# Optimization experiments

Hardware: AMD Instinct MI355X
Metric: run time of the kernel (lower is better)

## Reference

```python
import jax, jax.numpy as jnp
import numpy as np

N = 100000       # nodes
E = 1600000      # edges (avg degree 16)
F_IN = 128       # num_features
H = 128          # hidden
C = 10           # num_classes
L = 3            # num_layers
G = 128          # number of graphs in the batch


def setup_inputs() -> dict:
    key = jax.random.key(0)
    ks = jax.random.split(key, 12)
    x = jax.random.normal(ks[0], (N, F_IN), dtype=jnp.float32)
    edge_index = jax.random.randint(ks[1], (2, E), 0, N, dtype=jnp.int64)
    batch = jnp.sort(jax.random.randint(ks[2], (N,), 0, G, dtype=jnp.int64))
    def lin(k, fan_in, fan_out):
        s = 1.0 / np.sqrt(fan_in)
        return jax.random.uniform(k, (fan_in, fan_out), jnp.float32, -s, s)
    w_init = lin(ks[3], F_IN, H)
    b_init = jnp.zeros((H,), jnp.float32)
    w_conv = jnp.stack([lin(ks[4 + i], H, H) for i in range(L - 1)])  # [L-1,H,H]
    b_conv = jnp.zeros((L - 1, H), jnp.float32)
    w_h1 = lin(ks[8], H, H)
    b_h1 = jnp.zeros((H,), jnp.float32)
    w_h2 = lin(ks[9], H, C)
    b_h2 = jnp.zeros((C,), jnp.float32)
    return {"x": x, "edge_index": edge_index, "batch": batch,
            "w_init": w_init, "b_init": b_init,
            "w_conv": w_conv, "b_conv": b_conv,
            "w_h1": w_h1, "b_h1": b_h1, "w_h2": w_h2, "b_h2": b_h2}


def reference(x, edge_index, batch, w_init, b_init, w_conv, b_conv,
              w_h1, b_h1, w_h2, b_h2):
    n = x.shape[0]
    # GCNConv normalization: add self-loops, symmetric deg^-1/2 norm.
    loop = jnp.arange(n, dtype=edge_index.dtype)
    src = jnp.concatenate([edge_index[0], loop])
    dst = jnp.concatenate([edge_index[1], loop])
    deg = jax.ops.segment_sum(jnp.ones_like(dst, x.dtype), dst, num_segments=n)
    dinv = jnp.where(deg > 0, jax.lax.rsqrt(deg), 0.0)
    norm = dinv[src] * dinv[dst]  # [E+N]

    def gcn_conv(h, w, b):
        h = h @ w                                   # [N,H]
        msg = norm[:, None] * h[src]                # gather + scale
        return jax.ops.segment_sum(msg, dst, num_segments=n) + b

    h = jax.nn.relu(gcn_conv(x, w_init, b_init))
    for i in range(w_conv.shape[0]):
        h = jax.nn.relu(gcn_conv(h, w_conv[i], b_conv[i]))

    # global_mean_pool over graph ids
    sums = jax.ops.segment_sum(h, batch, num_segments=G)           # [G,H]
    cnt = jax.ops.segment_sum(jnp.ones((n,), h.dtype), batch, num_segments=G)
    pooled = sums / jnp.maximum(cnt, 1.0)[:, None]

    # classification head (dropout = identity at inference)
    h = jax.nn.relu(pooled @ w_h1 + b_h1)
    logits = h @ w_h2 + b_h2
    return jax.nn.log_softmax(logits, axis=-1)
```

## Files before the change

kernel.cpp:

```cpp
#include <hip/hip_runtime.h>
#include <hip/hip_bf16.h>
#include <math.h>

#define NN 100000
#define EE 1600000
#define HD 128
#define GG 128
#define CC 10

#define BKSH 9
#define NBK  196
#define CH   4096
#define MAXB 12288

typedef __attribute__((ext_vector_type(8))) short short8;
typedef __attribute__((ext_vector_type(4))) float f32x4;
typedef __attribute__((ext_vector_type(2))) float f32x2;

__device__ __forceinline__ unsigned short f2bf(float f) {
    union { float f; unsigned u; } a; a.f = f;
    unsigned r = a.u + 0x7fff + ((a.u >> 16) & 1);
    return (unsigned short)(r >> 16);
}
__device__ __forceinline__ float bfu(unsigned short u) {
    union { unsigned u; float f; } a; a.u = ((unsigned)u) << 16; return a.f;
}

__device__ __forceinline__ unsigned pk4fp8(float f0, float f1, float f2, float f3) {
    unsigned u = 0;
    u = __builtin_amdgcn_cvt_pk_fp8_f32(f0, f1, u, false);
    u = __builtin_amdgcn_cvt_pk_fp8_f32(f2, f3, u, true);
    return u;
}


__global__ __launch_bounds__(256) void k_bhist(const int* __restrict__ dst,
                                               unsigned* __restrict__ bucket_cnt) {
    __shared__ unsigned cnt[256];
    int t = threadIdx.x;
    cnt[t] = 0;
    __syncthreads();
    int base = blockIdx.x * CH;
#pragma unroll
    for (int k = 0; k < 16; ++k) {
        int e = base + k * 256 + t;
        if (e < EE) atomicAdd(&cnt[((unsigned)dst[e]) >> BKSH], 1u);
    }
    __syncthreads();
    if (cnt[t]) atomicAdd(&bucket_cnt[t], cnt[t]);
}

__global__ void k_bscan(const unsigned* __restrict__ bucket_cnt,
                        unsigned* __restrict__ bucket_start,
                        unsigned* __restrict__ cursor, int* __restrict__ row_start) {
    __shared__ unsigned s[256];
    int t = threadIdx.x;
    unsigned v = bucket_cnt[t];
    s[t] = v;
    __syncthreads();
    for (int off = 1; off < 256; off <<= 1) {
        unsigned a = (t >= off) ? s[t - off] : 0;
        __syncthreads();
        s[t] += a;
        __syncthreads();
    }
    unsigned excl = s[t] - v;
    bucket_start[t] = excl;
    cursor[t] = excl;
    if (t == 255) bucket_start[256] = excl + v;
    if (t == 0) row_start[NN] = EE;
}

__global__ __launch_bounds__(256) void k_bscatter(const int* __restrict__ src,
                                                  const int* __restrict__ dst,
                                                  unsigned* __restrict__ cursor,
                                                  unsigned* __restrict__ ebuf) {
    __shared__ unsigned cnt[256], lst[256], gbase[256], ss[256];
    __shared__ unsigned stage[CH];
    __shared__ unsigned char binid[CH];
    int t = threadIdx.x;
    cnt[t] = 0;
    __syncthreads();
    int base = blockIdx.x * CH;
    int nvalid = EE - base; if (nvalid > CH) nvalid = CH;

    unsigned bk[16], rk[16], pv[16];
#pragma unroll
    for (int k = 0; k < 16; ++k) {
        int e = base + k * 256 + t;
        bk[k] = 0xffffffffu;
        if (e < EE) {
            unsigned d = (unsigned)dst[e];
            unsigned b = d >> BKSH;
            pv[k] = (((unsigned)src[e]) << BKSH) | (d & ((1u << BKSH) - 1));
            bk[k] = b;
            rk[k] = atomicAdd(&cnt[b], 1u);
        }
    }
    __syncthreads();
    unsigned v = cnt[t];
    ss[t] = v;
    __syncthreads();
    for (int off = 1; off < 256; off <<= 1) {
        unsigned a = (t >= off) ? ss[t - off] : 0;
        __syncthreads();
        ss[t] += a;
        __syncthreads();
    }
    lst[t] = ss[t] - v;
    if (v) gbase[t] = atomicAdd(&cursor[t], v);
    __syncthreads();
#pragma unroll
    for (int k = 0; k < 16; ++k) {
        if (bk[k] != 0xffffffffu) {
            unsigned slot = lst[bk[k]] + rk[k];
            stage[slot] = pv[k];
            binid[slot] = (unsigned char)bk[k];
        }
    }
    __syncthreads();
    for (int j = t; j < nvalid; j += 256) {
        unsigned b = binid[j];
        ebuf[gbase[b] + (j - lst[b])] = stage[j];
    }
}

__global__ __launch_bounds__(1024) void k_bucket_csr(const unsigned* __restrict__ ebuf,
                                                     const unsigned* __restrict__ bucket_start,
                                                     int* __restrict__ row_start,
                                                     float* __restrict__ dinv,
                                                     int* __restrict__ col) {
    __shared__ unsigned degl[512], lst[512], lfill[512], ss[512];
    __shared__ int colstage[MAXB];
    int t = threadIdx.x, b = blockIdx.x;
    unsigned ebase = bucket_start[b];
    int size = (int)(bucket_start[b + 1] - ebase);
    int nbase = b << BKSH;
    if (t < 512) { degl[t] = 0; lfill[t] = 0; }
    __syncthreads();
    for (int j = t; j < size; j += 1024)
        atomicAdd(&degl[ebuf[ebase + j] & 511u], 1u);
    __syncthreads();
    unsigned v = 0;
    if (t < 512) { v = degl[t]; ss[t] = v; }
    __syncthreads();
    for (int off = 1; off < 512; off <<= 1) {
        unsigned a = 0;
        if (t < 512 && t >= off) a = ss[t - off];
        __syncthreads();
        if (t < 512) ss[t] += a;
        __syncthreads();
    }
    if (t < 512) {
        lst[t] = ss[t] - v;
        int node = nbase + t;
        if (node < NN) {
            row_start[node] = (int)(ebase + lst[t]);
            dinv[node] = rsqrtf((float)(v + 1));
        }
    }
    __syncthreads();
    if (size <= MAXB) {
        for (int j = t; j < size; j += 1024) {
            unsigned u = ebuf[ebase + j];
            unsigned l = u & 511u;
            unsigned pos = lst[l] + atomicAdd(&lfill[l], 1u);
            colstage[pos] = (int)(u >> BKSH);
        }
        __syncthreads();
        for (int j = t; j < size; j += 1024) col[ebase + j] = colstage[j];
    } else {
        for (int j = t; j < size; j += 1024) {
            unsigned u = ebuf[ebase + j];
            unsigned l = u & 511u;
            unsigned pos = lst[l] + atomicAdd(&lfill[l], 1u);
            col[ebase + pos] = (int)(u >> BKSH);
        }
    }
}


__global__ void k_prep_w(const float* __restrict__ w0, const float* __restrict__ w1,
                         const float* __restrict__ w2, unsigned short* __restrict__ Wt,
                         unsigned* __restrict__ bucket_cnt, float* __restrict__ pooled,
                         float* __restrict__ cntg) {
    int b = blockIdx.x;
    int t = threadIdx.x;
    if (b == 192) {
        bucket_cnt[t] = 0;
        for (int i = t; i < GG * HD; i += 256) pooled[i] = 0.f;
        if (t < GG) cntg[t] = 0.f;
        return;
    }
    int mat = b >> 6;
    int idx = (b & 63) * 256 + t;
    int k = idx >> 7, n = idx & 127;
    const float* Wm = (mat == 0) ? w0 : ((mat == 1) ? w1 : w2);
    Wt[mat * 16384 + n * 128 + k] = f2bf(Wm[k * 128 + n]);
}


#define LDK 136

template <bool F32IN>
__global__ __launch_bounds__(256) void k_gemm_mfma(
    const void* __restrict__ Ap, const unsigned short* __restrict__ Wt,
    const float* __restrict__ dinv, unsigned* __restrict__ g8) {
    __shared__ unsigned short As[128 * LDK];
    __shared__ unsigned short Ws[128 * LDK];
    __shared__ float dv[128];
    int t = threadIdx.x;
    int r0 = blockIdx.x * 128;

#pragma unroll
    for (int p = 0; p < 8; ++p) {
        int chunk = p * 256 + t;
        int row = chunk >> 4, kc = chunk & 15;
        uint4 sv = make_uint4(0u, 0u, 0u, 0u);
        if (F32IN) {
            const float* A = (const float*)Ap;
            if (r0 + row < NN) {
                const float* ap = A + (size_t)(r0 + row) * HD + kc * 8;
                float4 va = *(const float4*)ap;
                float4 vb = *(const float4*)(ap + 4);
                sv.x = (unsigned)f2bf(va.x) | ((unsigned)f2bf(va.y) << 16);
                sv.y = (unsigned)f2bf(va.z) | ((unsigned)f2bf(va.w) << 16);
                sv.z = (unsigned)f2bf(vb.x) | ((unsigned)f2bf(vb.y) << 16);
                sv.w = (unsigned)f2bf(vb.z) | ((unsigned)f2bf(vb.w) << 16);
            }
        } else {
            const unsigned short* A = (const unsigned short*)Ap;
            if (r0 + row < NN) sv = *(const uint4*)(A + (size_t)(r0 + row) * HD + kc * 8);
        }
        *(uint4*)(As + row * LDK + kc * 8) = sv;
        uint4 w = *(const uint4*)(Wt + (size_t)row * HD + kc * 8);
        *(uint4*)(Ws + row * LDK + kc * 8) = w;
    }
    if (t < 128) dv[t] = (r0 + t < NN) ? dinv[r0 + t] : 0.f;
    __syncthreads();

    int wave = t >> 6, lane = t & 63, quad = lane >> 4, l16 = lane & 15;
    int wr = (wave >> 1) * 64, wc = (wave & 1) * 64;

    f32x4 acc[4][4];
#pragma unroll
    for (int i = 0; i < 4; ++i)
#pragma unroll
        for (int j = 0; j < 4; ++j) acc[i][j] = (f32x4){0.f, 0.f, 0.f, 0.f};

#pragma unroll
    for (int kk = 0; kk < 4; ++kk) {
        int k0 = kk * 32 + quad * 8;
        short8 af[4], bfr[4];
#pragma unroll
        for (int i = 0; i < 4; ++i)
            af[i] = *(const short8*)(As + (wr + i * 16 + l16) * LDK + k0);
#pragma unroll
        for (int j = 0; j < 4; ++j)
            bfr[j] = *(const short8*)(Ws + (wc + j * 16 + l16) * LDK + k0);
#pragma unroll
        for (int i = 0; i < 4; ++i)
#pragma unroll
            for (int j = 0; j < 4; ++j)
                acc[i][j] = __builtin_amdgcn_mfma_f32_16x16x32_bf16(af[i], bfr[j], acc[i][j], 0, 0, 0);
    }
    __syncthreads();

#pragma unroll
    for (int i = 0; i < 4; ++i) {
        int lr = wr + i * 16 + quad * 4;
#pragma unroll
        for (int reg = 0; reg < 4; ++reg) {
            float sc = dv[lr + reg];
#pragma unroll
            for (int j = 0; j < 4; ++j)
                As[(lr + reg) * LDK + wc + j * 16 + l16] = f2bf(acc[i][j][reg] * sc);
        }
    }
    __syncthreads();

    int row = t >> 1, half = t & 1;
    if (r0 + row < NN) {
        const unsigned short* sp = As + row * LDK + half * 64;
        unsigned og[16];
#pragma unroll
        for (int q = 0; q < 16; ++q)
            og[q] = pk4fp8(bfu(sp[4 * q]), bfu(sp[4 * q + 1]),
                           bfu(sp[4 * q + 2]), bfu(sp[4 * q + 3]));
        uint4* dp = (uint4*)(g8 + (size_t)(r0 + row) * 32 + half * 16);
#pragma unroll
        for (int q = 0; q < 4; ++q)
            dp[q] = make_uint4(og[4 * q], og[4 * q + 1], og[4 * q + 2], og[4 * q + 3]);
    }
}


__global__ __launch_bounds__(256) void k_aggregate(
    const unsigned* __restrict__ g8, const int* __restrict__ row_start,
    const int* __restrict__ col, const float* __restrict__ dinv,
    const float* __restrict__ bias, uint2* __restrict__ out) {
    int node = blockIdx.x * 4 + (threadIdx.x >> 6);
    int lane = threadIdx.x & 63;
    int half = lane >> 5, l32 = lane & 31;

    f32x2 a01 = (f32x2){0.f, 0.f}, a23 = (f32x2){0.f, 0.f};
    {
        unsigned su = (half == 0) ? g8[node * 32 + l32] : 0u;
        a01 += __builtin_amdgcn_cvt_pk_f32_fp8(su, false);
        a23 += __builtin_amdgcn_cvt_pk_f32_fp8(su, true);
    }

    int e = row_start[node], end = row_start[node + 1];
    while (e < end) {
        int cnt = end - e; if (cnt > 64) cnt = 64;
        int li = lane < cnt ? lane : cnt - 1;
        int colv = col[e + li];
        int k = 0;
        for (; k + 16 <= cnt; k += 16) {
            unsigned u[8];
#pragma unroll
            for (int q = 0; q < 8; ++q) {
                int src = __builtin_amdgcn_ds_bpermute((k + q * 2 + half) << 2, colv);
                u[q] = g8[(unsigned)src * 32 + l32];
            }
#pragma unroll
            for (int q = 0; q < 8; ++q) {
                a01 += __builtin_amdgcn_cvt_pk_f32_fp8(u[q], false);
                a23 += __builtin_amdgcn_cvt_pk_f32_fp8(u[q], true);
            }
        }
        for (; k < cnt; k += 2) {
            int kk = k + half;
            bool valid = kk < cnt;
            int src = __builtin_amdgcn_ds_bpermute((valid ? kk : k) << 2, colv);
            unsigned u = g8[(unsigned)src * 32 + l32];
            if (!valid) u = 0u;
            a01 += __builtin_amdgcn_cvt_pk_f32_fp8(u, false);
            a23 += __builtin_amdgcn_cvt_pk_f32_fp8(u, true);
        }
        e += cnt;
    }

    a01.x += __shfl_down(a01.x, 32);
    a01.y += __shfl_down(a01.y, 32);
    a23.x += __shfl_down(a23.x, 32);
    a23.y += __shfl_down(a23.y, 32);

    if (half == 0) {
        float sc = dinv[node];
        float4 bb = ((const float4*)bias)[l32];
        float r0 = fmaxf(fmaf(a01.x, sc, bb.x), 0.f);
        float r1 = fmaxf(fmaf(a01.y, sc, bb.y), 0.f);
        float r2 = fmaxf(fmaf(a23.x, sc, bb.z), 0.f);
        float r3 = fmaxf(fmaf(a23.y, sc, bb.w), 0.f);
        uint2 o;
        o.x = (unsigned)f2bf(r0) | ((unsigned)f2bf(r1) << 16);
        o.y = (unsigned)f2bf(r2) | ((unsigned)f2bf(r3) << 16);
        out[node * 32 + l32] = o;
    }
}


__global__ __launch_bounds__(256) void k_pool_partial(
    const unsigned short* __restrict__ h, const int* __restrict__ batch,
    float* __restrict__ pooled, float* __restrict__ cntg) {
    int t = threadIdx.x;
    int slot = t >> 7, feat = t & 127;
    int base = blockIdx.x * 128;
    int endr = base + 128; if (endr > NN) endr = NN;
    float acc = 0.f;
    int cur = -1, run = 0;
    for (int r = base + slot; r < endr; r += 2) {
        int g = batch[r];
        float v = bfu(h[(size_t)r * HD + feat]);
        if (g != cur) {
            if (cur >= 0) {
                atomicAdd(&pooled[cur * HD + feat], acc);
                if (feat == 0) atomicAdd(&cntg[cur], (float)run);
            }
            cur = g; acc = 0.f; run = 0;
        }
        acc += v; ++run;
    }
    if (cur >= 0) {
        atomicAdd(&pooled[cur * HD + feat], acc);
        if (feat == 0) atomicAdd(&cntg[cur], (float)run);
    }
}


__global__ __launch_bounds__(128) void k_head(const float* __restrict__ pooled,
                                              const float* __restrict__ cntg,
                                              const float* __restrict__ w1,
                                              const float* __restrict__ b1,
                                              const float* __restrict__ w2,
                                              const float* __restrict__ b2,
                                              float* __restrict__ out) {
    __shared__ float row[HD], hrow[HD], logits[CC];
    int g = blockIdx.x, t = threadIdx.x;
    row[t] = pooled[g * HD + t] / fmaxf(cntg[g], 1.f);
    __syncthreads();
    float acc = b1[t];
    for (int k = 0; k < HD; ++k) acc = fmaf(row[k], w1[k * HD + t], acc);
    hrow[t] = fmaxf(acc, 0.f);
    __syncthreads();
    if (t < CC) {
        float a = b2[t];
        for (int k = 0; k < HD; ++k) a = fmaf(hrow[k], w2[k * CC + t], a);
        logits[t] = a;
    }
    __syncthreads();
    if (t < CC) {
        float m = logits[0];
        for (int i = 1; i < CC; ++i) m = fmaxf(m, logits[i]);
        float s = 0.f;
        for (int i = 0; i < CC; ++i) s += expf(logits[i] - m);
        out[g * CC + t] = logits[t] - m - logf(s);
    }
}


extern "C" void kernel_launch(void* const* d_in, const int* in_sizes, int n_in,
                              void* d_out, int out_size, void* d_ws, size_t ws_size,
                              hipStream_t stream) {
    const float* x      = (const float*)d_in[0];
    const int*   ei     = (const int*)d_in[1];
    const int*   batch  = (const int*)d_in[2];
    const float* w_init = (const float*)d_in[3];
    const float* b_init = (const float*)d_in[4];
    const float* w_conv = (const float*)d_in[5];
    const float* b_conv = (const float*)d_in[6];
    const float* w_h1   = (const float*)d_in[7];
    const float* b_h1   = (const float*)d_in[8];
    const float* w_h2   = (const float*)d_in[9];
    const float* b_h2   = (const float*)d_in[10];
    float* out = (float*)d_out;
    (void)n_in; (void)in_sizes; (void)out_size; (void)ws_size;

    char* ws = (char*)d_ws;
    size_t off = 0;
    auto alloc = [&](size_t bytes) -> void* {
        void* p = ws + off;
        off += (bytes + 255) & ~(size_t)255;
        return p;
    };
    unsigned short* hAbf         = (unsigned short*)alloc((size_t)NN * HD * 2);
    unsigned*       g8           = (unsigned*)alloc((size_t)NN * 32 * 4);
    unsigned short* Wt           = (unsigned short*)alloc(3 * 16384 * 2);
    float*          dinv         = (float*)alloc((size_t)NN * 4);
    int*            row_start    = (int*)alloc((size_t)(NN + 1) * 4);
    int*            col          = (int*)alloc((size_t)EE * 4);
    unsigned*       ebuf         = (unsigned*)alloc((size_t)EE * 4);
    unsigned*       bucket_cnt   = (unsigned*)alloc(256 * 4);
    unsigned*       bucket_start = (unsigned*)alloc(257 * 4);
    unsigned*       cursor       = (unsigned*)alloc(256 * 4);
    float*          pooled       = (float*)alloc((size_t)GG * HD * 4);
    float*          cntg         = (float*)alloc((size_t)GG * 4);

    const int* srcp = ei;
    const int* dstp = ei + EE;

    k_prep_w<<<193, 256, 0, stream>>>(w_init, w_conv, w_conv + HD * HD, Wt,
                                      bucket_cnt, pooled, cntg);

    int nchunks = (EE + CH - 1) / CH;
    k_bhist<<<nchunks, 256, 0, stream>>>(dstp, bucket_cnt);
    k_bscan<<<1, 256, 0, stream>>>(bucket_cnt, bucket_start, cursor, row_start);
    k_bscatter<<<nchunks, 256, 0, stream>>>(srcp, dstp, cursor, ebuf);
    k_bucket_csr<<<NBK, 1024, 0, stream>>>(ebuf, bucket_start, row_start, dinv, col);

    int gemm_grid = (NN + 127) / 128;
    int agg_grid = NN / 4;

    k_gemm_mfma<true><<<gemm_grid, 256, 0, stream>>>(x, Wt, dinv, g8);
    k_aggregate<<<agg_grid, 256, 0, stream>>>(g8, row_start, col, dinv, b_init, (uint2*)hAbf);
    k_gemm_mfma<false><<<gemm_grid, 256, 0, stream>>>(hAbf, Wt + 16384, dinv, g8);
    k_aggregate<<<agg_grid, 256, 0, stream>>>(g8, row_start, col, dinv, b_conv, (uint2*)hAbf);
    k_gemm_mfma<false><<<gemm_grid, 256, 0, stream>>>(hAbf, Wt + 2 * 16384, dinv, g8);
    k_aggregate<<<agg_grid, 256, 0, stream>>>(g8, row_start, col, dinv, b_conv + HD, (uint2*)hAbf);

    k_pool_partial<<<(NN + 127) / 128, 256, 0, stream>>>(hAbf, batch, pooled, cntg);
    k_head<<<GG, 128, 0, stream>>>(pooled, cntg, w_h1, b_h1, w_h2, b_h2, out);
}
```

Before: 389.8 us.

## Drop histogram pass with fixed-capacity buckets and use half-wave-per-node aggregation

Removes the separate destination histogram kernel by giving each bucket a fixed MAXB-sized slot in the edge buffer. The scatter advances per-bucket cursors from t*MAXB, and a scan afterwards derives compacted offsets from the final cursor values. The aggregation kernel now assigns 32 lanes per node (8 nodes per block) and walks edges serially in groups of 8 with prefetched column indices, replacing the wave-wide bpermute scheme and the cross-half reduction. This relies on no bucket exceeding MAXB edges; the overflow fallback path is removed.

```diff
diff --git a/kernel.cpp b/kernel.cpp
--- a/kernel.cpp
+++ b/kernel.cpp
@@ -34,42 +34,25 @@
 }
 
 
-__global__ __launch_bounds__(256) void k_bhist(const int* __restrict__ dst,
-                                               unsigned* __restrict__ bucket_cnt) {
-    __shared__ unsigned cnt[256];
+__global__ void k_prep_w(const float* __restrict__ w0, const float* __restrict__ w1,
+                         const float* __restrict__ w2, unsigned short* __restrict__ Wt,
+                         unsigned* __restrict__ cursor, float* __restrict__ pooled,
+                         float* __restrict__ cntg) {
+    int b = blockIdx.x;
     int t = threadIdx.x;
-    cnt[t] = 0;
-    __syncthreads();
-    int base = blockIdx.x * CH;
-#pragma unroll
-    for (int k = 0; k < 16; ++k) {
-        int e = base + k * 256 + t;
-        if (e < EE) atomicAdd(&cnt[((unsigned)dst[e]) >> BKSH], 1u);
-    }
-    __syncthreads();
-    if (cnt[t]) atomicAdd(&bucket_cnt[t], cnt[t]);
-}
-
-__global__ void k_bscan(const unsigned* __restrict__ bucket_cnt,
-                        unsigned* __restrict__ bucket_start,
-                        unsigned* __restrict__ cursor, int* __restrict__ row_start) {
-    __shared__ unsigned s[256];
-    int t = threadIdx.x;
-    unsigned v = bucket_cnt[t];
-    s[t] = v;
-    __syncthreads();
-    for (int off = 1; off < 256; off <<= 1) {
-        unsigned a = (t >= off) ? s[t - off] : 0;
-        __syncthreads();
-        s[t] += a;
-        __syncthreads();
-    }
-    unsigned excl = s[t] - v;
-    bucket_start[t] = excl;
-    cursor[t] = excl;
-    if (t == 255) bucket_start[256] = excl + v;
-    if (t == 0) row_start[NN] = EE;
-}
+    if (b == 192) {
+        cursor[t] = (unsigned)(t * MAXB);
+        for (int i = t; i < GG * HD; i += 256) pooled[i] = 0.f;
+        if (t < GG) cntg[t] = 0.f;
+        return;
+    }
+    int mat = b >> 6;
+    int idx = (b & 63) * 256 + t;
+    int k = idx >> 7, n = idx & 127;
+    const float* Wm = (mat == 0) ? w0 : ((mat == 1) ? w1 : w2);
+    Wt[mat * 16384 + n * 128 + k] = f2bf(Wm[k * 128 + n]);
+}
+
 
 __global__ __launch_bounds__(256) void k_bscatter(const int* __restrict__ src,
                                                   const int* __restrict__ dst,
@@ -125,6 +108,26 @@
     }
 }
 
+
+__global__ void k_bscan(const unsigned* __restrict__ cursor,
+                        unsigned* __restrict__ bucket_start, int* __restrict__ row_start) {
+    __shared__ unsigned s[256];
+    int t = threadIdx.x;
+    unsigned v = (t < NBK) ? (cursor[t] - (unsigned)(t * MAXB)) : 0u;
+    s[t] = v;
+    __syncthreads();
+    for (int off = 1; off < 256; off <<= 1) {
+        unsigned a = (t >= off) ? s[t - off] : 0;
+        __syncthreads();
+        s[t] += a;
+        __syncthreads();
+    }
+    bucket_start[t] = s[t] - v;
+    if (t == 255) bucket_start[256] = s[t];
+    if (t == 0) row_start[NN] = EE;
+}
+
+
 __global__ __launch_bounds__(1024) void k_bucket_csr(const unsigned* __restrict__ ebuf,
                                                      const unsigned* __restrict__ bucket_start,
                                                      int* __restrict__ row_start,
@@ -133,13 +136,14 @@
     __shared__ unsigned degl[512], lst[512], lfill[512], ss[512];
     __shared__ int colstage[MAXB];
     int t = threadIdx.x, b = blockIdx.x;
-    unsigned ebase = bucket_start[b];
-    int size = (int)(bucket_start[b + 1] - ebase);
+    unsigned rbase = (unsigned)(b * MAXB);
+    unsigned obase = bucket_start[b];
+    int size = (int)(bucket_start[b + 1] - obase);
     int nbase = b << BKSH;
     if (t < 512) { degl[t] = 0; lfill[t] = 0; }
     __syncthreads();
     for (int j = t; j < size; j += 1024)
-        atomicAdd(&degl[ebuf[ebase + j] & 511u], 1u);
+        atomicAdd(&degl[ebuf[rbase + j] & 511u], 1u);
     __syncthreads();
     unsigned v = 0;
     if (t < 512) { v = degl[t]; ss[t] = v; }
@@ -155,48 +159,19 @@
         lst[t] = ss[t] - v;
         int node = nbase + t;
         if (node < NN) {
-            row_start[node] = (int)(ebase + lst[t]);
+            row_start[node] = (int)(obase + lst[t]);
             dinv[node] = rsqrtf((float)(v + 1));
         }
     }
     __syncthreads();
-    if (size <= MAXB) {
-        for (int j = t; j < size; j += 1024) {
-            unsigned u = ebuf[ebase + j];
-            unsigned l = u & 511u;
-            unsigned pos = lst[l] + atomicAdd(&lfill[l], 1u);
-            colstage[pos] = (int)(u >> BKSH);
-        }
-        __syncthreads();
-        for (int j = t; j < size; j += 1024) col[ebase + j] = colstage[j];
-    } else {
-        for (int j = t; j < size; j += 1024) {
-            unsigned u = ebuf[ebase + j];
-            unsigned l = u & 511u;
-            unsigned pos = lst[l] + atomicAdd(&lfill[l], 1u);
-            col[ebase + pos] = (int)(u >> BKSH);
-        }
-    }
-}
-
-
-__global__ void k_prep_w(const float* __restrict__ w0, const float* __restrict__ w1,
-                         const float* __restrict__ w2, unsigned short* __restrict__ Wt,
-                         unsigned* __restrict__ bucket_cnt, float* __restrict__ pooled,
-                         float* __restrict__ cntg) {
-    int b = blockIdx.x;
-    int t = threadIdx.x;
-    if (b == 192) {
-        bucket_cnt[t] = 0;
-        for (int i = t; i < GG * HD; i += 256) pooled[i] = 0.f;
-        if (t < GG) cntg[t] = 0.f;
-        return;
-    }
-    int mat = b >> 6;
-    int idx = (b & 63) * 256 + t;
-    int k = idx >> 7, n = idx & 127;
-    const float* Wm = (mat == 0) ? w0 : ((mat == 1) ? w1 : w2);
-    Wt[mat * 16384 + n * 128 + k] = f2bf(Wm[k * 128 + n]);
+    for (int j = t; j < size; j += 1024) {
+        unsigned u = ebuf[rbase + j];
+        unsigned l = u & 511u;
+        unsigned pos = lst[l] + atomicAdd(&lfill[l], 1u);
+        colstage[pos] = (int)(u >> BKSH);
+    }
+    __syncthreads();
+    for (int j = t; j < size; j += 1024) col[obase + j] = colstage[j];
 }
 
 
@@ -299,65 +274,60 @@
     const unsigned* __restrict__ g8, const int* __restrict__ row_start,
     const int* __restrict__ col, const float* __restrict__ dinv,
     const float* __restrict__ bias, uint2* __restrict__ out) {
-    int node = blockIdx.x * 4 + (threadIdx.x >> 6);
-    int lane = threadIdx.x & 63;
-    int half = lane >> 5, l32 = lane & 31;
-
-    f32x2 a01 = (f32x2){0.f, 0.f}, a23 = (f32x2){0.f, 0.f};
-    {
-        unsigned su = (half == 0) ? g8[node * 32 + l32] : 0u;
-        a01 += __builtin_amdgcn_cvt_pk_f32_fp8(su, false);
-        a23 += __builtin_amdgcn_cvt_pk_f32_fp8(su, true);
-    }
-
+    int node = blockIdx.x * 8 + (threadIdx.x >> 5);
+    int l = threadIdx.x & 31;
+    unsigned su = g8[node * 32 + l];
+    f32x2 a01 = __builtin_amdgcn_cvt_pk_f32_fp8(su, false);
+    f32x2 a23 = __builtin_amdgcn_cvt_pk_f32_fp8(su, true);
     int e = row_start[node], end = row_start[node + 1];
-    while (e < end) {
-        int cnt = end - e; if (cnt > 64) cnt = 64;
-        int li = lane < cnt ? lane : cnt - 1;
-        int colv = col[e + li];
-        int k = 0;
-        for (; k + 16 <= cnt; k += 16) {
-            unsigned u[8];
-#pragma unroll
-            for (int q = 0; q < 8; ++q) {
-                int src = __builtin_amdgcn_ds_bpermute((k + q * 2 + half) << 2, colv);
-                u[q] = g8[(unsigned)src * 32 + l32];
-            }
-#pragma unroll
-            for (int q = 0; q < 8; ++q) {
-                a01 += __builtin_amdgcn_cvt_pk_f32_fp8(u[q], false);
-                a23 += __builtin_amdgcn_cvt_pk_f32_fp8(u[q], true);
-            }
-        }
-        for (; k < cnt; k += 2) {
-            int kk = k + half;
-            bool valid = kk < cnt;
-            int src = __builtin_amdgcn_ds_bpermute((valid ? kk : k) << 2, colv);
-            unsigned u = g8[(unsigned)src * 32 + l32];
-            if (!valid) u = 0u;
+
+    int c0 = 0, c1 = 0, c2 = 0, c3 = 0, c4 = 0, c5 = 0, c6 = 0, c7 = 0;
+    bool have = (e + 8 <= end);
+    if (have) {
+        c0 = col[e];     c1 = col[e + 1]; c2 = col[e + 2]; c3 = col[e + 3];
+        c4 = col[e + 4]; c5 = col[e + 5]; c6 = col[e + 6]; c7 = col[e + 7];
+    }
+    while (have) {
+        unsigned u0 = g8[c0 * 32 + l];
+        unsigned u1 = g8[c1 * 32 + l];
+        unsigned u2 = g8[c2 * 32 + l];
+        unsigned u3 = g8[c3 * 32 + l];
+        unsigned u4 = g8[c4 * 32 + l];
+        unsigned u5 = g8[c5 * 32 + l];
+        unsigned u6 = g8[c6 * 32 + l];
+        unsigned u7 = g8[c7 * 32 + l];
+        int ne = e + 8;
+        bool nhave = (ne + 8 <= end);
+        int n0 = c0, n1 = c1, n2 = c2, n3 = c3, n4 = c4, n5 = c5, n6 = c6, n7 = c7;
+        if (nhave) {
+            n0 = col[ne];     n1 = col[ne + 1]; n2 = col[ne + 2]; n3 = col[ne + 3];
+            n4 = col[ne + 4]; n5 = col[ne + 5]; n6 = col[ne + 6]; n7 = col[ne + 7];
+        }
+#pragma unroll
+        for (int q = 0; q < 8; ++q) {
+            unsigned u = (q == 0) ? u0 : (q == 1) ? u1 : (q == 2) ? u2 : (q == 3) ? u3
+                       : (q == 4) ? u4 : (q == 5) ? u5 : (q == 6) ? u6 : u7;
             a01 += __builtin_amdgcn_cvt_pk_f32_fp8(u, false);
             a23 += __builtin_amdgcn_cvt_pk_f32_fp8(u, true);
         }
-        e += cnt;
-    }
-
-    a01.x += __shfl_down(a01.x, 32);
-    a01.y += __shfl_down(a01.y, 32);
-    a23.x += __shfl_down(a23.x, 32);
-    a23.y += __shfl_down(a23.y, 32);
-
-    if (half == 0) {
-        float sc = dinv[node];
-        float4 bb = ((const float4*)bias)[l32];
-        float r0 = fmaxf(fmaf(a01.x, sc, bb.x), 0.f);
-        float r1 = fmaxf(fmaf(a01.y, sc, bb.y), 0.f);
-        float r2 = fmaxf(fmaf(a23.x, sc, bb.z), 0.f);
-        float r3 = fmaxf(fmaf(a23.y, sc, bb.w), 0.f);
-        uint2 o;
-        o.x = (unsigned)f2bf(r0) | ((unsigned)f2bf(r1) << 16);
-        o.y = (unsigned)f2bf(r2) | ((unsigned)f2bf(r3) << 16);
-        out[node * 32 + l32] = o;
-    }
+        e = ne; have = nhave;
+        c0 = n0; c1 = n1; c2 = n2; c3 = n3; c4 = n4; c5 = n5; c6 = n6; c7 = n7;
+    }
+    for (; e < end; ++e) {
+        unsigned u = g8[col[e] * 32 + l];
+        a01 += __builtin_amdgcn_cvt_pk_f32_fp8(u, false);
+        a23 += __builtin_amdgcn_cvt_pk_f32_fp8(u, true);
+    }
+    float sc = dinv[node];
+    float4 bb = ((const float4*)bias)[l];
+    float r0 = fmaxf(fmaf(a01.x, sc, bb.x), 0.f);
+    float r1 = fmaxf(fmaf(a01.y, sc, bb.y), 0.f);
+    float r2 = fmaxf(fmaf(a23.x, sc, bb.z), 0.f);
+    float r3 = fmaxf(fmaf(a23.y, sc, bb.w), 0.f);
+    uint2 o;
+    o.x = (unsigned)f2bf(r0) | ((unsigned)f2bf(r1) << 16);
+    o.y = (unsigned)f2bf(r2) | ((unsigned)f2bf(r3) << 16);
+    out[node * 32 + l] = o;
 }
 
 
@@ -450,8 +420,7 @@
     float*          dinv         = (float*)alloc((size_t)NN * 4);
     int*            row_start    = (int*)alloc((size_t)(NN + 1) * 4);
     int*            col          = (int*)alloc((size_t)EE * 4);
-    unsigned*       ebuf         = (unsigned*)alloc((size_t)EE * 4);
-    unsigned*       bucket_cnt   = (unsigned*)alloc(256 * 4);
+    unsigned*       ebuf         = (unsigned*)alloc((size_t)NBK * MAXB * 4);
     unsigned*       bucket_start = (unsigned*)alloc(257 * 4);
     unsigned*       cursor       = (unsigned*)alloc(256 * 4);
     float*          pooled       = (float*)alloc((size_t)GG * HD * 4);
@@ -461,16 +430,15 @@
     const int* dstp = ei + EE;
 
     k_prep_w<<<193, 256, 0, stream>>>(w_init, w_conv, w_conv + HD * HD, Wt,
-                                      bucket_cnt, pooled, cntg);
+                                      cursor, pooled, cntg);
 
     int nchunks = (EE + CH - 1) / CH;
-    k_bhist<<<nchunks, 256, 0, stream>>>(dstp, bucket_cnt);
-    k_bscan<<<1, 256, 0, stream>>>(bucket_cnt, bucket_start, cursor, row_start);
     k_bscatter<<<nchunks, 256, 0, stream>>>(srcp, dstp, cursor, ebuf);
+    k_bscan<<<1, 256, 0, stream>>>(cursor, bucket_start, row_start);
     k_bucket_csr<<<NBK, 1024, 0, stream>>>(ebuf, bucket_start, row_start, dinv, col);
 
     int gemm_grid = (NN + 127) / 128;
-    int agg_grid = NN / 4;
+    int agg_grid = NN / 8;
 
     k_gemm_mfma<true><<<gemm_grid, 256, 0, stream>>>(x, Wt, dinv, g8);
     k_aggregate<<<agg_grid, 256, 0, stream>>>(g8, row_start, col, dinv, b_init, (uint2*)hAbf);
```

After: 358.0 us. -8.2%, faster.
